# Performance work log

Hardware: AMD Instinct MI355X
Metric: run time of the kernel (lower is better)

Reference implementation:

```python
import jax, jax.numpy as jnp
import numpy as np

N = 262144   # nodes
E = 1048576  # edges (avg degree 4)
DIN = 64     # input node features
H = 128      # hidden channels
DE = 32      # edge feature dim
EPS = 1e-5


def setup_inputs() -> dict:
    key = jax.random.key(0)
    ks = jax.random.split(key, 12)
    s = 0.05
    return {
        "x": jax.random.normal(ks[0], (N, DIN), jnp.float32),
        "edge_attr": jax.random.normal(ks[1], (E, DE), jnp.float32),
        "W_enter": jax.random.normal(ks[2], (H, DIN), jnp.float32) * s,
        "b_enter": jnp.zeros((H,), jnp.float32),
        "W1": jax.random.normal(ks[3], (H, H + DE), jnp.float32) * s,
        "att_l": jax.random.normal(ks[4], (H,), jnp.float32) * s,
        "att_r": jax.random.normal(ks[5], (H,), jnp.float32) * s,
        "W2": jax.random.normal(ks[6], (H, H), jnp.float32) * s,
        "b_conv": jnp.zeros((H,), jnp.float32),
        "W_ih": jax.random.normal(ks[7], (3 * H, H), jnp.float32) * s,
        "W_hh": jax.random.normal(ks[8], (3 * H, H), jnp.float32) * s,
        "b_ih": jnp.zeros((3 * H,), jnp.float32),
        "b_hh": jnp.zeros((3 * H,), jnp.float32),
        "edge_index": jax.random.randint(ks[9], (2, E), 0, N, jnp.int32),
    }


def _segment_softmax(logits, seg, num_segments):
    m = jax.ops.segment_max(logits, seg, num_segments=num_segments)
    e = jnp.exp(logits - m[seg])
    d = jax.ops.segment_sum(e, seg, num_segments=num_segments)
    return e / d[seg]


def reference(x, edge_attr, W_enter, b_enter, W1, att_l, att_r, W2, b_conv,
              W_ih, W_hh, b_ih, b_hh, edge_index):
    n = x.shape[0]
    src, dst = edge_index[0], edge_index[1]  # x_j = x[src], aggregate to dst

    # lin_enter + leaky_relu
    x = jax.nn.leaky_relu(x @ W_enter.T + b_enter)

    # Edge2dConv message: leaky_relu(lin1([x_j, edge_attr]))
    m = jax.nn.leaky_relu(jnp.concatenate([x[src], edge_attr], axis=-1) @ W1.T)  # [E,H]
    alpha = jax.nn.leaky_relu(m @ att_l + x[dst] @ att_r)  # [E]
    alpha = _segment_softmax(alpha, dst, n)
    msg = (m @ W2.T) * alpha[:, None]
    out = jax.ops.segment_sum(msg, dst, num_segments=n) + b_conv

    # elu, then GRUCell(h_in=out_elu, hidden=x)
    h = jax.nn.elu(out)
    gi = h @ W_ih.T + b_ih
    gh = x @ W_hh.T + b_hh
    ir, iz, inn = jnp.split(gi, 3, axis=-1)
    hr, hz, hn = jnp.split(gh, 3, axis=-1)
    r = jax.nn.sigmoid(ir + hr)
    z = jax.nn.sigmoid(iz + hz)
    ncand = jnp.tanh(inn + r * hn)
    x = jax.nn.relu((1.0 - z) * ncand + z * x)

    # layer_norm (no affine)
    mu = jnp.mean(x, axis=-1, keepdims=True)
    var = jnp.mean(jnp.square(x - mu), axis=-1, keepdims=True)
    return (x - mu) / jnp.sqrt(var + EPS)
```

## Files before the change

### kernel.cpp

```cpp
#include <hip/hip_runtime.h>
#include <stdint.h>

#define HD  128
#define DIN 64
#define DE  32

typedef unsigned int u32; typedef unsigned short u16; typedef unsigned char u8;
typedef long i64_;
typedef short s16x8 __attribute__((ext_vector_type(8)));
typedef float f32x4 __attribute__((ext_vector_type(4)));
typedef float f32x2 __attribute__((ext_vector_type(2)));

#define MFMA16(a,b,c)  __builtin_amdgcn_mfma_f32_16x16x32_bf16((a),(b),(c),0,0,0)
#define MFMAF8(a,b,c)  __builtin_amdgcn_mfma_f32_16x16x32_fp8_fp8((a),(b),(c),0,0,0)

__device__ __forceinline__ float lrelu(float x){ return x > 0.f ? x : 0.01f*x; }
__device__ __forceinline__ float sigmoidf_(float x){ return 1.f/(1.f + __expf(-x)); }
__device__ __forceinline__ float tanhf_(float x){
    float t = fminf(fmaxf(x, -15.f), 15.f);
    float e = __expf(2.f*t);
    return (e - 1.f)/(e + 1.f);
}
__device__ __forceinline__ float eluf_(float x){ return x > 0.f ? x : expm1f(x); }

__device__ __forceinline__ u16 f32_to_bf16(float x){
    u32 u = __float_as_uint(x);
    u += 0x7FFFu + ((u >> 16) & 1u);
    return (u16)(u >> 16);
}
__device__ __forceinline__ float bf16lo(u32 u){ return __uint_as_float((u & 0xFFFFu) << 16); }
__device__ __forceinline__ float bf16hi(u32 u){ return __uint_as_float(u & 0xFFFF0000u); }
__device__ __forceinline__ float bf16f(u16 h){ return __uint_as_float(((u32)h) << 16); }
__device__ __forceinline__ u32 pk2(float a, float b){
    return (u32)f32_to_bf16(a) | ((u32)f32_to_bf16(b) << 16);
}
__device__ __forceinline__ u8 hw_f8(float v){
    return (u8)__builtin_amdgcn_cvt_pk_fp8_f32(v, v, 0, false);
}
__device__ __forceinline__ u32 hw_f8x4(float a, float b, float c, float d){
    u32 r = (u32)__builtin_amdgcn_cvt_pk_fp8_f32(a, b, 0, false);
    r = (u32)__builtin_amdgcn_cvt_pk_fp8_f32(c, d, (int)r, true);
    return r;
}
__device__ __forceinline__ f32x2 hw_f8_dec2(u32 u){
    return __builtin_amdgcn_cvt_pk_f32_fp8((int)u, false);
}
__device__ __forceinline__ f32x2 hw_f8_dec2_hi(u32 u){
    return __builtin_amdgcn_cvt_pk_f32_fp8((int)u, true);
}

__device__ __forceinline__ float wave_max(float v){
    #pragma unroll
    for (int o = 32; o > 0; o >>= 1) v = fmaxf(v, __shfl_xor(v, o, 64));
    return v;
}
__device__ __forceinline__ float wave_sum(float v){
    #pragma unroll
    for (int o = 32; o > 0; o >>= 1) v += __shfl_xor(v, o, 64);
    return v;
}

__global__ void k_prep(const float* __restrict__ W1, const float* __restrict__ W2,
                       const float* __restrict__ Went,
                       const float* __restrict__ Wih, const float* __restrict__ Whh,
                       u16* __restrict__ W1b, u16* __restrict__ W2b,
                       u16* __restrict__ Wentb, u8* __restrict__ Bgf8)
{
    int i = blockIdx.x*256 + threadIdx.x;
    if (i < 20480){ W1b[i] = f32_to_bf16(W1[i]); return; }
    i -= 20480;
    if (i < 16384){ W2b[i] = f32_to_bf16(W2[i]); return; }
    i -= 16384;
    if (i < 8192){ Wentb[i] = f32_to_bf16(Went[i]); return; }
    i -= 8192;
    if (i < 131072){
        int col = i >> 8, k = i & 255;
        int g = col >> 7, j = col & 127;
        float v;
        if      (g == 0) v = (k < 128) ? Wih[j*128 + k]        : Whh[j*128 + k - 128];
        else if (g == 1) v = (k < 128) ? Wih[(128+j)*128 + k]  : Whh[(128+j)*128 + k - 128];
        else if (g == 2) v = (k < 128) ? Wih[(256+j)*128 + k]  : 0.f;
        else             v = (k < 128) ? 0.f                   : Whh[(256+j)*128 + k - 128];
        Bgf8[i] = hw_f8(v);
    }
}

__global__ __launch_bounds__(256, 4) void k_enter_mfma(
    const float* __restrict__ x, const u16* __restrict__ Wb, const float* __restrict__ be,
    const float* __restrict__ att_r, u16* __restrict__ xeb, u8* __restrict__ Agru,
    float* __restrict__ r_out, int N)
{
    __shared__ __align__(16) u8 sA[64*144];
    __shared__ __align__(16) u8 sO[64*272];
    int t = threadIdx.x, w = t >> 6, lane = t & 63, l15 = lane & 15, l4 = lane >> 4;
    int tile = blockIdx.x;

    s16x8 bfr[2][2];
    #pragma unroll
    for (int kf = 0; kf < 2; ++kf)
        #pragma unroll
        for (int cf = 0; cf < 2; ++cf)
            bfr[kf][cf] = *(const s16x8*)(Wb + (size_t)(w*32 + cf*16 + l15)*64 + kf*32 + l4*8);

    int el = t >> 2, q = t & 3;
    size_t n = (size_t)tile*64 + el;
    {
        const float4* xs = (const float4*)(x + n*64 + q*16);
        float4 f0 = xs[0], f1 = xs[1], f2 = xs[2], f3 = xs[3];
        uint4 o0, o1;
        o0.x = pk2(f0.x,f0.y); o0.y = pk2(f0.z,f0.w); o0.z = pk2(f1.x,f1.y); o0.w = pk2(f1.z,f1.w);
        o1.x = pk2(f2.x,f2.y); o1.y = pk2(f2.z,f2.w); o1.z = pk2(f3.x,f3.y); o1.w = pk2(f3.z,f3.w);
        *(uint4*)(sA + el*144 + q*32)      = o0;
        *(uint4*)(sA + el*144 + q*32 + 16) = o1;
    }
    __syncthreads();

    f32x4 acc[4][2];
    #pragma unroll
    for (int rf = 0; rf < 4; ++rf){ acc[rf][0] = (f32x4)0.f; acc[rf][1] = (f32x4)0.f; }
    #pragma unroll
    for (int kf = 0; kf < 2; ++kf){
        s16x8 a[4];
        #pragma unroll
        for (int rf = 0; rf < 4; ++rf)
            a[rf] = *(const s16x8*)(sA + (rf*16 + l15)*144 + kf*64 + l4*16);
        #pragma unroll
        for (int rf = 0; rf < 4; ++rf){
            acc[rf][0] = MFMA16(a[rf], bfr[kf][0], acc[rf][0]);
            acc[rf][1] = MFMA16(a[rf], bfr[kf][1], acc[rf][1]);
        }
    }
    float b0 = be[w*32 + l15], b1 = be[w*32 + 16 + l15];
    #pragma unroll
    for (int rf = 0; rf < 4; ++rf)
        #pragma unroll
        for (int r = 0; r < 4; ++r){
            int row = rf*16 + l4*4 + r;
            *(u16*)(sO + row*272 + (w*32 + l15)*2)      = f32_to_bf16(lrelu(acc[rf][0][r] + b0));
            *(u16*)(sO + row*272 + (w*32 + 16 + l15)*2) = f32_to_bf16(lrelu(acc[rf][1][r] + b1));
        }
    __syncthreads();

    float dot = 0.f;
    #pragma unroll
    for (int i = 0; i < 4; ++i){
        uint4 v = *(const uint4*)(sO + el*272 + q*64 + 16*i);
        ((uint4*)xeb)[n*16 + q*4 + i] = v;
        float f0 = bf16lo(v.x), f1 = bf16hi(v.x), f2 = bf16lo(v.y), f3 = bf16hi(v.y);
        float f4 = bf16lo(v.z), f5 = bf16hi(v.z), f6 = bf16lo(v.w), f7 = bf16hi(v.w);
        const float* al = att_r + q*32 + 8*i;
        dot = fmaf(f0, al[0], dot); dot = fmaf(f1, al[1], dot);
        dot = fmaf(f2, al[2], dot); dot = fmaf(f3, al[3], dot);
        dot = fmaf(f4, al[4], dot); dot = fmaf(f5, al[5], dot);
        dot = fmaf(f6, al[6], dot); dot = fmaf(f7, al[7], dot);
        uint2 p; p.x = hw_f8x4(f0, f1, f2, f3); p.y = hw_f8x4(f4, f5, f6, f7);
        *(uint2*)(Agru + n*256 + 128 + q*32 + i*8) = p;
    }
    dot += __shfl_xor(dot, 1); dot += __shfl_xor(dot, 2);
    if (q == 0) r_out[n] = dot;
}

__global__ void k_hist(const int* __restrict__ dst, int* __restrict__ deg, int E){
    int e = blockIdx.x*256 + threadIdx.x;
    if (e < E) atomicAdd(&deg[dst[e]], 1);
}
__global__ __launch_bounds__(256) void k_scan_a(
    const int* __restrict__ deg, int* __restrict__ rs, int* __restrict__ btot, int N)
{
    __shared__ int sd[256];
    int b = blockIdx.x, t = threadIdx.x;
    int base = b*1024 + t*4;
    int d0 = deg[base], d1 = deg[base+1], d2 = deg[base+2], d3 = deg[base+3];
    int s = d0 + d1 + d2 + d3;
    sd[t] = s; __syncthreads();
    for (int o = 1; o < 256; o <<= 1){
        int v = (t >= o) ? sd[t-o] : 0;
        __syncthreads();
        sd[t] += v;
        __syncthreads();
    }
    int ex = sd[t] - s;
    rs[base]   = ex;
    rs[base+1] = ex + d0;
    rs[base+2] = ex + d0 + d1;
    rs[base+3] = ex + d0 + d1 + d2;
    if (t == 0) btot[b] = sd[255];
}
__global__ __launch_bounds__(256) void k_scan_b(const int* __restrict__ btot, int* __restrict__ bbase){
    __shared__ int sd[256];
    int t = threadIdx.x;
    int s = btot[t];
    sd[t] = s; __syncthreads();
    for (int o = 1; o < 256; o <<= 1){
        int v = (t >= o) ? sd[t-o] : 0;
        __syncthreads();
        sd[t] += v;
        __syncthreads();
    }
    bbase[t] = sd[t] - s;
}
__global__ void k_scan_c(int* __restrict__ rs, const int* __restrict__ bbase, int N, int E){
    int i = blockIdx.x*256 + threadIdx.x;
    if (i < N) rs[i] += bbase[i >> 10];
    if (i == 0) rs[N] = E;
}
__global__ void k_scatter(const int* __restrict__ dst, const int* __restrict__ rs,
                          int* __restrict__ cnt, int* __restrict__ epos, int E){
    int e = blockIdx.x*256 + threadIdx.x;
    if (e >= E) return;
    int d = dst[e];
    int pos = rs[d] + atomicAdd(&cnt[d], 1);
    epos[e] = pos;
}

__global__ __launch_bounds__(512, 4) void k_edge_mfma(
    const u16* __restrict__ xeb, const float* __restrict__ ea,
    const u16* __restrict__ W1b, const float* __restrict__ att_l,
    const int* __restrict__ src, const int* __restrict__ epos,
    u8* __restrict__ m, float* __restrict__ alpha, int ntiles, int E)
{
    __shared__ __align__(16) u8 sA[64*336];
    __shared__ __align__(16) u8 sM[64*144];
    int t = threadIdx.x, w = t >> 6, lane = t & 63, l15 = lane & 15, l4 = lane >> 4;

    s16x8 bfr[5];
    #pragma unroll
    for (int kf = 0; kf < 5; ++kf)
        bfr[kf] = *(const s16x8*)(W1b + (size_t)(w*16 + l15)*160 + kf*32 + l4*8);

    int el = t >> 3, q = t & 7;
    int stride = gridDim.x;
    int tile = blockIdx.x;

    uint4 cx0, cx1;
    u32 ce0, ce1;
    int pe = 0;
    {
        int e = tile*64 + el;
        if (tile < ntiles && e < E){
            int sn = src[e];
            const uint4* xs = (const uint4*)xeb + (size_t)sn*16 + q*2;
            cx0 = xs[0]; cx1 = xs[1];
            float4 f = *(const float4*)(ea + (size_t)e*32 + q*4);
            ce0 = pk2(f.x, f.y); ce1 = pk2(f.z, f.w);
            pe  = epos[e];
        }
    }

    int ptile = -1;
    int pe_prev = 0;

    for (; tile < ntiles; tile += stride){
        int e = tile*64 + el;
        if (e < E){
            uint4* d = (uint4*)(sA + el*336 + q*32);
            d[0] = cx0; d[1] = cx1;
            *(u32*)(sA + el*336 + 256 + q*8)     = ce0;
            *(u32*)(sA + el*336 + 256 + q*8 + 4) = ce1;
        }
        int pe_cur = pe;

        int nt = tile + stride;
        if (nt < ntiles){
            int e2 = nt*64 + el;
            if (e2 < E){
                int sn = src[e2];
                const uint4* xs = (const uint4*)xeb + (size_t)sn*16 + q*2;
                cx0 = xs[0]; cx1 = xs[1];
                float4 f = *(const float4*)(ea + (size_t)e2*32 + q*4);
                ce0 = pk2(f.x, f.y); ce1 = pk2(f.z, f.w);
                pe  = epos[e2];
            }
        }

        if (ptile >= 0){
            int ep = ptile*64 + el;
            if (ep < E){
                uint4 v = *(const uint4*)(sM + el*144 + q*16);
                ((uint4*)m)[(size_t)pe_prev*8 + q] = v;
                u32 ws[4] = {v.x, v.y, v.z, v.w};
                float dotv = 0.f;
                #pragma unroll
                for (int i = 0; i < 4; ++i){
                    f32x2 fa = hw_f8_dec2(ws[i]);
                    f32x2 fb = hw_f8_dec2_hi(ws[i]);
                    const float* al = att_l + q*16 + i*4;
                    dotv = fmaf(fa.x, al[0], dotv); dotv = fmaf(fa.y, al[1], dotv);
                    dotv = fmaf(fb.x, al[2], dotv); dotv = fmaf(fb.y, al[3], dotv);
                }
                dotv += __shfl_xor(dotv, 1); dotv += __shfl_xor(dotv, 2); dotv += __shfl_xor(dotv, 4);
                if (q == 0) alpha[pe_prev] = dotv;
            }
        }
        __syncthreads();

        f32x4 acc[4];
        #pragma unroll
        for (int rf = 0; rf < 4; ++rf) acc[rf] = (f32x4)0.f;
        #pragma unroll
        for (int kf = 0; kf < 5; ++kf){
            s16x8 a[4];
            #pragma unroll
            for (int rf = 0; rf < 4; ++rf)
                a[rf] = *(const s16x8*)(sA + (rf*16 + l15)*336 + kf*64 + l4*16);
            #pragma unroll
            for (int rf = 0; rf < 4; ++rf)
                acc[rf] = MFMA16(a[rf], bfr[kf], acc[rf]);
        }

        int col = w*16 + l15;
        #pragma unroll
        for (int rf = 0; rf < 4; ++rf)
            #pragma unroll
            for (int r = 0; r < 4; ++r){
                int row = rf*16 + l4*4 + r;
                sM[row*144 + col] = hw_f8(lrelu(acc[rf][r]));
            }
        __syncthreads();

        ptile = tile; pe_prev = pe_cur;
    }

    if (ptile >= 0){
        int ep = ptile*64 + el;
        if (ep < E){
            uint4 v = *(const uint4*)(sM + el*144 + q*16);
            ((uint4*)m)[(size_t)pe_prev*8 + q] = v;
            u32 ws[4] = {v.x, v.y, v.z, v.w};
            float dotv = 0.f;
            #pragma unroll
            for (int i = 0; i < 4; ++i){
                f32x2 fa = hw_f8_dec2(ws[i]);
                f32x2 fb = hw_f8_dec2_hi(ws[i]);
                const float* al = att_l + q*16 + i*4;
                dotv = fmaf(fa.x, al[0], dotv); dotv = fmaf(fa.y, al[1], dotv);
                dotv = fmaf(fb.x, al[2], dotv); dotv = fmaf(fb.y, al[3], dotv);
            }
            dotv += __shfl_xor(dotv, 1); dotv += __shfl_xor(dotv, 2); dotv += __shfl_xor(dotv, 4);
            if (q == 0) alpha[pe_prev] = dotv;
        }
    }
}

__global__ __launch_bounds__(512, 4) void k_aggconv(
    const int* __restrict__ rs, const float* __restrict__ alpha, const u8* __restrict__ m,
    const float* __restrict__ r_dst,
    const u16* __restrict__ W2b, const float* __restrict__ bc,
    u8* __restrict__ Agru, int N)
{
    __shared__ __align__(16) u8 sA[64*272];
    __shared__ __align__(16) u8 sO[64*272];
    int t = threadIdx.x, w = t >> 6, lane = t & 63, l15 = lane & 15, l4 = lane >> 4;
    int tile = blockIdx.x;

    s16x8 bfr[4];
    #pragma unroll
    for (int kf = 0; kf < 4; ++kf)
        bfr[kf] = *(const s16x8*)(W2b + (size_t)(w*16 + l15)*128 + kf*32 + l4*8);

    #pragma unroll 1
    for (int i = 0; i < 8; ++i){
        int nloc = w*8 + i;
        int n = tile*64 + nloc;
        int s = rs[n], tend = rs[n+1];
        int deg = tend - s;
        float rn = r_dst[n];
        float ax = 0.f, ay = 0.f;
        if (deg > 0 && deg <= 64){
            float av = -1e38f;
            if (lane < deg) av = lrelu(alpha[s + lane] + rn);
            float mx = wave_max(av);
            float ev = (lane < deg) ? __expf(av - mx) : 0.f;
            float ssum = wave_sum(ev);
            float wreg = ev / ssum;
            int k = 0;
            for (; k + 2 <= deg; k += 2){
                float w0 = __shfl(wreg, k);
                float w1 = __shfl(wreg, k + 1);
                u32 u0 = *(const u16*)(m + (size_t)(s + k)*HD + 2*lane);
                u32 u1 = *(const u16*)(m + (size_t)(s + k + 1)*HD + 2*lane);
                f32x2 f0 = hw_f8_dec2(u0);
                f32x2 f1 = hw_f8_dec2(u1);
                ax = fmaf(w0, f0.x, ax); ay = fmaf(w0, f0.y, ay);
                ax = fmaf(w1, f1.x, ax); ay = fmaf(w1, f1.y, ay);
            }
            if (k < deg){
                float w0 = __shfl(wreg, k);
                u32 u0 = *(const u16*)(m + (size_t)(s + k)*HD + 2*lane);
                f32x2 f0 = hw_f8_dec2(u0);
                ax = fmaf(w0, f0.x, ax); ay = fmaf(w0, f0.y, ay);
            }
        } else if (deg > 64){
            float mx = -1e38f;
            for (int k = lane; k < deg; k += 64) mx = fmaxf(mx, lrelu(alpha[s + k] + rn));
            mx = wave_max(mx);
            float ssum = 0.f;
            for (int k = lane; k < deg; k += 64) ssum += __expf(lrelu(alpha[s + k] + rn) - mx);
            ssum = wave_sum(ssum);
            float inv = 1.f / ssum;
            for (int k = 0; k < deg; ++k){
                float wgt = __expf(lrelu(alpha[s + k] + rn) - mx) * inv;
                u32 u0 = *(const u16*)(m + (size_t)(s + k)*HD + 2*lane);
                f32x2 f0 = hw_f8_dec2(u0);
                ax = fmaf(wgt, f0.x, ax);
                ay = fmaf(wgt, f0.y, ay);
            }
        }
        *(u32*)(sA + nloc*272 + lane*4) = pk2(ax, ay);
    }
    __syncthreads();

    f32x4 acc[4];
    #pragma unroll
    for (int rf = 0; rf < 4; ++rf) acc[rf] = (f32x4)0.f;
    #pragma unroll
    for (int kf = 0; kf < 4; ++kf){
        s16x8 av[4];
        #pragma unroll
        for (int rf = 0; rf < 4; ++rf)
            av[rf] = *(const s16x8*)(sA + (rf*16 + l15)*272 + kf*64 + l4*16);
        #pragma unroll
        for (int rf = 0; rf < 4; ++rf)
            acc[rf] = MFMA16(av[rf], bfr[kf], acc[rf]);
    }
    float b0 = bc[w*16 + l15];
    #pragma unroll
    for (int rf = 0; rf < 4; ++rf)
        #pragma unroll
        for (int r = 0; r < 4; ++r){
            int row = rf*16 + l4*4 + r;
            *(u16*)(sO + row*272 + (w*16 + l15)*2) = f32_to_bf16(eluf_(acc[rf][r] + b0));
        }
    __syncthreads();

    {
        int el = t >> 3, q = t & 7;
        size_t n = (size_t)tile*64 + el;
        uint4 v0 = *(const uint4*)(sO + el*272 + q*32);
        uint4 v1 = *(const uint4*)(sO + el*272 + q*32 + 16);
        uint4 p;
        p.x = hw_f8x4(bf16lo(v0.x), bf16hi(v0.x), bf16lo(v0.y), bf16hi(v0.y));
        p.y = hw_f8x4(bf16lo(v0.z), bf16hi(v0.z), bf16lo(v0.w), bf16hi(v0.w));
        p.z = hw_f8x4(bf16lo(v1.x), bf16hi(v1.x), bf16lo(v1.y), bf16hi(v1.y));
        p.w = hw_f8x4(bf16lo(v1.z), bf16hi(v1.z), bf16lo(v1.w), bf16hi(v1.w));
        *(uint4*)(Agru + n*256 + q*16) = p;
    }
}

__global__ __launch_bounds__(512, 4) void k_gru_mfma(
    const u8* __restrict__ Agru, const u16* __restrict__ xeb, const u8* __restrict__ Bgf8,
    const float* __restrict__ bih, const float* __restrict__ bhh,
    float* __restrict__ out, int N, int ntiles)
{
    __shared__ __align__(16) u8 sA[32*272];
    __shared__ __align__(16) u8 sX[32*272];
    __shared__ __align__(16) float sOut[32*132];
    int t = threadIdx.x, w = t >> 6, lane = t & 63, l15 = lane & 15, l4 = lane >> 4;

    i64_ bfr0[8], bfr1[8], bfr2[4], bfr3[4];
    {
        int jc = w*16 + l15;
        #pragma unroll
        for (int kf = 0; kf < 8; ++kf){
            bfr0[kf] = *(const i64_*)(Bgf8 + (size_t)(jc)*256       + kf*32 + l4*8);
            bfr1[kf] = *(const i64_*)(Bgf8 + (size_t)(128 + jc)*256 + kf*32 + l4*8);
        }
        #pragma unroll
        for (int kf = 0; kf < 4; ++kf){
            bfr2[kf] = *(const i64_*)(Bgf8 + (size_t)(256 + jc)*256 + kf*32 + l4*8);
            bfr3[kf] = *(const i64_*)(Bgf8 + (size_t)(384 + jc)*256 + (kf+4)*32 + l4*8);
        }
    }
    int j = w*16 + l15;
    float rb = bih[j] + bhh[j];
    float zb = bih[128 + j] + bhh[128 + j];
    float ib = bih[256 + j];
    float hb = bhh[256 + j];

    int el = t >> 4, part = t & 15;
    int stride = gridDim.x;
    int tile = blockIdx.x;
    uint4 pa, px;
    if (tile < ntiles){
        pa = *((const uint4*)Agru + ((size_t)tile*32 + el)*16 + part);
        px = *((const uint4*)xeb  + ((size_t)tile*32 + el)*16 + part);
    }

    for (; tile < ntiles; tile += stride){
        *(uint4*)(sA + el*272 + part*16) = pa;
        *(uint4*)(sX + el*272 + part*16) = px;
        __syncthreads();

        int nt = tile + stride;
        if (nt < ntiles){
            pa = *((const uint4*)Agru + ((size_t)nt*32 + el)*16 + part);
            px = *((const uint4*)xeb  + ((size_t)nt*32 + el)*16 + part);
        }

        f32x4 acc[2][4];
        #pragma unroll
        for (int rf = 0; rf < 2; ++rf)
            #pragma unroll
            for (int g = 0; g < 4; ++g) acc[rf][g] = (f32x4)0.f;
        #pragma unroll
        for (int kf = 0; kf < 8; ++kf){
            i64_ a0 = *(const i64_*)(sA + l15*272 + kf*32 + l4*8);
            i64_ a1 = *(const i64_*)(sA + (16 + l15)*272 + kf*32 + l4*8);
            acc[0][0] = MFMAF8(a0, bfr0[kf], acc[0][0]);
            acc[1][0] = MFMAF8(a1, bfr0[kf], acc[1][0]);
            acc[0][1] = MFMAF8(a0, bfr1[kf], acc[0][1]);
            acc[1][1] = MFMAF8(a1, bfr1[kf], acc[1][1]);
            if (kf < 4){
                acc[0][2] = MFMAF8(a0, bfr2[kf], acc[0][2]);
                acc[1][2] = MFMAF8(a1, bfr2[kf], acc[1][2]);
            } else {
                acc[0][3] = MFMAF8(a0, bfr3[kf-4], acc[0][3]);
                acc[1][3] = MFMAF8(a1, bfr3[kf-4], acc[1][3]);
            }
        }
        #pragma unroll
        for (int rf = 0; rf < 2; ++rf)
            #pragma unroll
            for (int r = 0; r < 4; ++r){
                int rl = rf*16 + l4*4 + r;
                float rr = sigmoidf_(acc[rf][0][r] + rb);
                float zz = sigmoidf_(acc[rf][1][r] + zb);
                float iv = acc[rf][2][r] + ib;
                float hv = acc[rf][3][r] + hb;
                float nc = tanhf_(iv + rr*hv);
                float xej = bf16f(*(const u16*)(sX + rl*272 + 2*j));
                float v = (1.f - zz)*nc + zz*xej;
                v = fmaxf(v, 0.f);
                sOut[rl*132 + j] = v;
            }
        __syncthreads();
        {
            int row = t >> 4, sub = t & 15;
            const float* rp = sOut + row*132 + sub*8;
            float v0 = rp[0], v1 = rp[1], v2 = rp[2], v3 = rp[3];
            float v4 = rp[4], v5 = rp[5], v6 = rp[6], v7 = rp[7];
            float s1 = v0+v1+v2+v3+v4+v5+v6+v7;
            float s2 = v0*v0+v1*v1+v2*v2+v3*v3+v4*v4+v5*v5+v6*v6+v7*v7;
            #pragma unroll
            for (int o = 1; o < 16; o <<= 1){ s1 += __shfl_xor(s1, o); s2 += __shfl_xor(s2, o); }
            float mu  = s1 * (1.f/128.f);
            float var = s2 * (1.f/128.f) - mu*mu;
            var = fmaxf(var, 0.f);
            float rsd = rsqrtf(var + 1e-5f);
            float* op = out + ((size_t)tile*32 + row)*128 + sub*8;
            float4 o0, o1;
            o0.x = (v0-mu)*rsd; o0.y = (v1-mu)*rsd; o0.z = (v2-mu)*rsd; o0.w = (v3-mu)*rsd;
            o1.x = (v4-mu)*rsd; o1.y = (v5-mu)*rsd; o1.z = (v6-mu)*rsd; o1.w = (v7-mu)*rsd;
            ((float4*)op)[0] = o0; ((float4*)op)[1] = o1;
        }
        __syncthreads();
    }
}

extern "C" void kernel_launch(void* const* d_in, const int* in_sizes, int n_in,
                              void* d_out, int out_size, void* d_ws, size_t ws_size,
                              hipStream_t stream)
{
    const float* x       = (const float*)d_in[0];
    const float* ea      = (const float*)d_in[1];
    const float* W_enter = (const float*)d_in[2];
    const float* b_enter = (const float*)d_in[3];
    const float* W1      = (const float*)d_in[4];
    const float* att_l   = (const float*)d_in[5];
    const float* att_r   = (const float*)d_in[6];
    const float* W2      = (const float*)d_in[7];
    const float* b_conv  = (const float*)d_in[8];
    const float* W_ih    = (const float*)d_in[9];
    const float* W_hh    = (const float*)d_in[10];
    const float* b_ih    = (const float*)d_in[11];
    const float* b_hh    = (const float*)d_in[12];
    const int*   eidx    = (const int*)d_in[13];

    int N = in_sizes[0] / DIN;
    int E = in_sizes[13] / 2;
    const int* src = eidx;
    const int* dst = eidx + E;
    float* out = (float*)d_out;

    size_t off = 0;
    char* base = (char*)d_ws;
    auto alloc = [&](size_t bytes) -> char* {
        char* p = base + off;
        off = (off + bytes + 255) & ~(size_t)255;
        return p;
    };
    u16*   xeb   = (u16*)  alloc((size_t)N*HD*2);
    u8*    Agru  = (u8*)   alloc((size_t)N*256);
    float* r_dst = (float*)alloc((size_t)N*4);
    float* alpha = (float*)alloc((size_t)E*4);
    int*   deg   = (int*)  alloc((size_t)N*4);
    int*   rs    = (int*)  alloc((size_t)(N+1)*4);
    int*   cnt   = (int*)  alloc((size_t)N*4);
    int*   epos  = (int*)  alloc((size_t)E*4);
    int*   btot  = (int*)  alloc(1024);
    int*   bbase = (int*)  alloc(1024);
    u16*   W1b   = (u16*)  alloc(20480*2);
    u16*   W2b   = (u16*)  alloc(16384*2);
    u16*   Wentb = (u16*)  alloc(8192*2);
    u8*    Bgf8  = (u8*)   alloc(131072);
    u8*    mbuf  = (u8*)   alloc((size_t)E*HD);

    int ntiles_n64 = N/64, ntiles_e = (E + 63)/64, ntiles_g = N/32;

    k_prep   <<<(176128+255)/256, 256, 0, stream>>>(W1, W2, W_enter, W_ih, W_hh, W1b, W2b, Wentb, Bgf8);
    hipMemsetAsync(deg, 0, (size_t)N*4, stream);
    hipMemsetAsync(cnt, 0, (size_t)N*4, stream);
    k_enter_mfma<<<ntiles_n64, 256, 0, stream>>>(x, Wentb, b_enter, att_r, xeb, Agru, r_dst, N);
    k_hist   <<<(E+255)/256, 256, 0, stream>>>(dst, deg, E);
    k_scan_a <<<N/1024, 256, 0, stream>>>(deg, rs, btot, N);
    k_scan_b <<<1, 256, 0, stream>>>(btot, bbase);
    k_scan_c <<<(N+255)/256, 256, 0, stream>>>(rs, bbase, N, E);
    k_scatter<<<(E+255)/256, 256, 0, stream>>>(dst, rs, cnt, epos, E);
    k_edge_mfma<<<1024, 512, 0, stream>>>(xeb, ea, W1b, att_l, src, epos,
                                          mbuf, alpha, ntiles_e, E);
    k_aggconv<<<ntiles_n64, 512, 0, stream>>>(rs, alpha, mbuf, r_dst, W2b, b_conv, Agru, N);
    k_gru_mfma  <<<1024, 512, 0, stream>>>(Agru, xeb, Bgf8, b_ih, b_hh, out, N, ntiles_g);
}
```

Before: 510.3 us.

## Fuse aggregation/conv kernel with GRU and layer-norm kernel

Merges the aggregation+W2 kernel with the GRU+layernorm kernel so the ELU output stays in shared memory as fp8 instead of going through a global Agru buffer. The enter kernel now writes a compact fp8 copy of x (Agx) that the fused kernel loads. This removes one kernel launch and a global write/read of the intermediate. In exchange the fused kernel holds more registers and shared memory (launch bounds lowered to 3), loses the persistent-grid prefetch the GRU kernel used, and reloads the GRU weights once per 64-node tile.

```diff
diff --git a/kernel.cpp b/kernel.cpp
--- a/kernel.cpp
+++ b/kernel.cpp
@@ -87,7 +87,7 @@
 
 __global__ __launch_bounds__(256, 4) void k_enter_mfma(
     const float* __restrict__ x, const u16* __restrict__ Wb, const float* __restrict__ be,
-    const float* __restrict__ att_r, u16* __restrict__ xeb, u8* __restrict__ Agru,
+    const float* __restrict__ att_r, u16* __restrict__ xeb, u8* __restrict__ Agx,
     float* __restrict__ r_out, int N)
 {
     __shared__ __align__(16) u8 sA[64*144];
@@ -154,7 +154,7 @@
         dot = fmaf(f4, al[4], dot); dot = fmaf(f5, al[5], dot);
         dot = fmaf(f6, al[6], dot); dot = fmaf(f7, al[7], dot);
         uint2 p; p.x = hw_f8x4(f0, f1, f2, f3); p.y = hw_f8x4(f4, f5, f6, f7);
-        *(uint2*)(Agru + n*256 + 128 + q*32 + i*8) = p;
+        *(uint2*)(Agx + n*128 + q*32 + i*8) = p;
     }
     dot += __shfl_xor(dot, 1); dot += __shfl_xor(dot, 2);
     if (q == 0) r_out[n] = dot;
@@ -342,21 +342,45 @@
     }
 }
 
-__global__ __launch_bounds__(512, 4) void k_aggconv(
+__global__ __launch_bounds__(512, 3) void k_aggconvgru(
     const int* __restrict__ rs, const float* __restrict__ alpha, const u8* __restrict__ m,
     const float* __restrict__ r_dst,
     const u16* __restrict__ W2b, const float* __restrict__ bc,
-    u8* __restrict__ Agru, int N)
+    const u8* __restrict__ Agx, const u16* __restrict__ xeb,
+    const u8* __restrict__ Bgf8,
+    const float* __restrict__ bih, const float* __restrict__ bhh,
+    float* __restrict__ out, int N)
 {
     __shared__ __align__(16) u8 sA[64*272];
     __shared__ __align__(16) u8 sO[64*272];
+    __shared__ __align__(16) float sOut[32*132];
     int t = threadIdx.x, w = t >> 6, lane = t & 63, l15 = lane & 15, l4 = lane >> 4;
     int tile = blockIdx.x;
 
-    s16x8 bfr[4];
+    i64_ bfr0[8], bfr1[8], bfr2[4], bfr3[4];
+    {
+        int jc = w*16 + l15;
+        #pragma unroll
+        for (int kf = 0; kf < 8; ++kf){
+            bfr0[kf] = *(const i64_*)(Bgf8 + (size_t)(jc)*256       + kf*32 + l4*8);
+            bfr1[kf] = *(const i64_*)(Bgf8 + (size_t)(128 + jc)*256 + kf*32 + l4*8);
+        }
+        #pragma unroll
+        for (int kf = 0; kf < 4; ++kf){
+            bfr2[kf] = *(const i64_*)(Bgf8 + (size_t)(256 + jc)*256 + kf*32 + l4*8);
+            bfr3[kf] = *(const i64_*)(Bgf8 + (size_t)(384 + jc)*256 + (kf+4)*32 + l4*8);
+        }
+    }
+    int j = w*16 + l15;
+    float rb = bih[j] + bhh[j];
+    float zb = bih[128 + j] + bhh[128 + j];
+    float ib = bih[256 + j];
+    float hb = bhh[256 + j];
+
+    s16x8 bfrW[4];
     #pragma unroll
     for (int kf = 0; kf < 4; ++kf)
-        bfr[kf] = *(const s16x8*)(W2b + (size_t)(w*16 + l15)*128 + kf*32 + l4*8);
+        bfrW[kf] = *(const s16x8*)(W2b + (size_t)(w*16 + l15)*128 + kf*32 + l4*8);
 
     #pragma unroll 1
     for (int i = 0; i < 8; ++i){
@@ -410,102 +434,54 @@
     }
     __syncthreads();
 
-    f32x4 acc[4];
-    #pragma unroll
-    for (int rf = 0; rf < 4; ++rf) acc[rf] = (f32x4)0.f;
-    #pragma unroll
-    for (int kf = 0; kf < 4; ++kf){
-        s16x8 av[4];
+    int grow = t >> 3, gq = t & 7;
+    size_t gn = (size_t)tile*64 + grow;
+    uint4 gxe  = *((const uint4*)(Agx + gn*128) + gq);
+    uint4 gxb0 = *((const uint4*)(xeb + gn*128) + gq*2);
+    uint4 gxb1 = *((const uint4*)(xeb + gn*128) + gq*2 + 1);
+
+    {
+        f32x4 acc[4];
+        #pragma unroll
+        for (int rf = 0; rf < 4; ++rf) acc[rf] = (f32x4)0.f;
+        #pragma unroll
+        for (int kf = 0; kf < 4; ++kf){
+            s16x8 av[4];
+            #pragma unroll
+            for (int rf = 0; rf < 4; ++rf)
+                av[rf] = *(const s16x8*)(sA + (rf*16 + l15)*272 + kf*64 + l4*16);
+            #pragma unroll
+            for (int rf = 0; rf < 4; ++rf)
+                acc[rf] = MFMA16(av[rf], bfrW[kf], acc[rf]);
+        }
+        float b0 = bc[w*16 + l15];
+        int col = w*16 + l15;
         #pragma unroll
         for (int rf = 0; rf < 4; ++rf)
-            av[rf] = *(const s16x8*)(sA + (rf*16 + l15)*272 + kf*64 + l4*16);
-        #pragma unroll
-        for (int rf = 0; rf < 4; ++rf)
-            acc[rf] = MFMA16(av[rf], bfr[kf], acc[rf]);
-    }
-    float b0 = bc[w*16 + l15];
-    #pragma unroll
-    for (int rf = 0; rf < 4; ++rf)
-        #pragma unroll
-        for (int r = 0; r < 4; ++r){
-            int row = rf*16 + l4*4 + r;
-            *(u16*)(sO + row*272 + (w*16 + l15)*2) = f32_to_bf16(eluf_(acc[rf][r] + b0));
-        }
+            #pragma unroll
+            for (int r = 0; r < 4; ++r){
+                int row = rf*16 + l4*4 + r;
+                sO[row*272 + col] = hw_f8(bf16f(f32_to_bf16(eluf_(acc[rf][r] + b0))));
+            }
+    }
+    *(uint4*)(sO + grow*272 + 128 + gq*16) = gxe;
     __syncthreads();
 
-    {
-        int el = t >> 3, q = t & 7;
-        size_t n = (size_t)tile*64 + el;
-        uint4 v0 = *(const uint4*)(sO + el*272 + q*32);
-        uint4 v1 = *(const uint4*)(sO + el*272 + q*32 + 16);
-        uint4 p;
-        p.x = hw_f8x4(bf16lo(v0.x), bf16hi(v0.x), bf16lo(v0.y), bf16hi(v0.y));
-        p.y = hw_f8x4(bf16lo(v0.z), bf16hi(v0.z), bf16lo(v0.w), bf16hi(v0.w));
-        p.z = hw_f8x4(bf16lo(v1.x), bf16hi(v1.x), bf16lo(v1.y), bf16hi(v1.y));
-        p.w = hw_f8x4(bf16lo(v1.z), bf16hi(v1.z), bf16lo(v1.w), bf16hi(v1.w));
-        *(uint4*)(Agru + n*256 + q*16) = p;
-    }
-}
-
-__global__ __launch_bounds__(512, 4) void k_gru_mfma(
-    const u8* __restrict__ Agru, const u16* __restrict__ xeb, const u8* __restrict__ Bgf8,
-    const float* __restrict__ bih, const float* __restrict__ bhh,
-    float* __restrict__ out, int N, int ntiles)
-{
-    __shared__ __align__(16) u8 sA[32*272];
-    __shared__ __align__(16) u8 sX[32*272];
-    __shared__ __align__(16) float sOut[32*132];
-    int t = threadIdx.x, w = t >> 6, lane = t & 63, l15 = lane & 15, l4 = lane >> 4;
-
-    i64_ bfr0[8], bfr1[8], bfr2[4], bfr3[4];
-    {
-        int jc = w*16 + l15;
+    *(uint4*)(sA + grow*272 + gq*32)      = gxb0;
+    *(uint4*)(sA + grow*272 + gq*32 + 16) = gxb1;
+    __syncthreads();
+
+    #pragma unroll 1
+    for (int hh = 0; hh < 2; ++hh){
+        f32x4 acc[2][4];
+        #pragma unroll
+        for (int rf = 0; rf < 2; ++rf)
+            #pragma unroll
+            for (int g = 0; g < 4; ++g) acc[rf][g] = (f32x4)0.f;
         #pragma unroll
         for (int kf = 0; kf < 8; ++kf){
-            bfr0[kf] = *(const i64_*)(Bgf8 + (size_t)(jc)*256       + kf*32 + l4*8);
-            bfr1[kf] = *(const i64_*)(Bgf8 + (size_t)(128 + jc)*256 + kf*32 + l4*8);
-        }
-        #pragma unroll
-        for (int kf = 0; kf < 4; ++kf){
-            bfr2[kf] = *(const i64_*)(Bgf8 + (size_t)(256 + jc)*256 + kf*32 + l4*8);
-            bfr3[kf] = *(const i64_*)(Bgf8 + (size_t)(384 + jc)*256 + (kf+4)*32 + l4*8);
-        }
-    }
-    int j = w*16 + l15;
-    float rb = bih[j] + bhh[j];
-    float zb = bih[128 + j] + bhh[128 + j];
-    float ib = bih[256 + j];
-    float hb = bhh[256 + j];
-
-    int el = t >> 4, part = t & 15;
-    int stride = gridDim.x;
-    int tile = blockIdx.x;
-    uint4 pa, px;
-    if (tile < ntiles){
-        pa = *((const uint4*)Agru + ((size_t)tile*32 + el)*16 + part);
-        px = *((const uint4*)xeb  + ((size_t)tile*32 + el)*16 + part);
-    }
-
-    for (; tile < ntiles; tile += stride){
-        *(uint4*)(sA + el*272 + part*16) = pa;
-        *(uint4*)(sX + el*272 + part*16) = px;
-        __syncthreads();
-
-        int nt = tile + stride;
-        if (nt < ntiles){
-            pa = *((const uint4*)Agru + ((size_t)nt*32 + el)*16 + part);
-            px = *((const uint4*)xeb  + ((size_t)nt*32 + el)*16 + part);
-        }
-
-        f32x4 acc[2][4];
-        #pragma unroll
-        for (int rf = 0; rf < 2; ++rf)
-            #pragma unroll
-            for (int g = 0; g < 4; ++g) acc[rf][g] = (f32x4)0.f;
-        #pragma unroll
-        for (int kf = 0; kf < 8; ++kf){
-            i64_ a0 = *(const i64_*)(sA + l15*272 + kf*32 + l4*8);
-            i64_ a1 = *(const i64_*)(sA + (16 + l15)*272 + kf*32 + l4*8);
+            i64_ a0 = *(const i64_*)(sO + (hh*32 + l15)*272 + kf*32 + l4*8);
+            i64_ a1 = *(const i64_*)(sO + (hh*32 + 16 + l15)*272 + kf*32 + l4*8);
             acc[0][0] = MFMAF8(a0, bfr0[kf], acc[0][0]);
             acc[1][0] = MFMAF8(a1, bfr0[kf], acc[1][0]);
             acc[0][1] = MFMAF8(a0, bfr1[kf], acc[0][1]);
@@ -528,7 +504,7 @@
                 float iv = acc[rf][2][r] + ib;
                 float hv = acc[rf][3][r] + hb;
                 float nc = tanhf_(iv + rr*hv);
-                float xej = bf16f(*(const u16*)(sX + rl*272 + 2*j));
+                float xej = bf16f(*(const u16*)(sA + (hh*32 + rl)*272 + 2*j));
                 float v = (1.f - zz)*nc + zz*xej;
                 v = fmaxf(v, 0.f);
                 sOut[rl*132 + j] = v;
@@ -547,7 +523,7 @@
             float var = s2 * (1.f/128.f) - mu*mu;
             var = fmaxf(var, 0.f);
             float rsd = rsqrtf(var + 1e-5f);
-            float* op = out + ((size_t)tile*32 + row)*128 + sub*8;
+            float* op = out + ((size_t)tile*64 + hh*32 + row)*128 + sub*8;
             float4 o0, o1;
             o0.x = (v0-mu)*rsd; o0.y = (v1-mu)*rsd; o0.z = (v2-mu)*rsd; o0.w = (v3-mu)*rsd;
             o1.x = (v4-mu)*rsd; o1.y = (v5-mu)*rsd; o1.z = (v6-mu)*rsd; o1.w = (v7-mu)*rsd;
@@ -590,7 +566,7 @@
         return p;
     };
     u16*   xeb   = (u16*)  alloc((size_t)N*HD*2);
-    u8*    Agru  = (u8*)   alloc((size_t)N*256);
+    u8*    Agx   = (u8*)   alloc((size_t)N*HD);
     float* r_dst = (float*)alloc((size_t)N*4);
     float* alpha = (float*)alloc((size_t)E*4);
     int*   deg   = (int*)  alloc((size_t)N*4);
@@ -605,12 +581,12 @@
     u8*    Bgf8  = (u8*)   alloc(131072);
     u8*    mbuf  = (u8*)   alloc((size_t)E*HD);
 
-    int ntiles_n64 = N/64, ntiles_e = (E + 63)/64, ntiles_g = N/32;
+    int ntiles_n64 = N/64, ntiles_e = (E + 63)/64;
 
     k_prep   <<<(176128+255)/256, 256, 0, stream>>>(W1, W2, W_enter, W_ih, W_hh, W1b, W2b, Wentb, Bgf8);
     hipMemsetAsync(deg, 0, (size_t)N*4, stream);
     hipMemsetAsync(cnt, 0, (size_t)N*4, stream);
-    k_enter_mfma<<<ntiles_n64, 256, 0, stream>>>(x, Wentb, b_enter, att_r, xeb, Agru, r_dst, N);
+    k_enter_mfma<<<ntiles_n64, 256, 0, stream>>>(x, Wentb, b_enter, att_r, xeb, Agx, r_dst, N);
     k_hist   <<<(E+255)/256, 256, 0, stream>>>(dst, deg, E);
     k_scan_a <<<N/1024, 256, 0, stream>>>(deg, rs, btot, N);
     k_scan_b <<<1, 256, 0, stream>>>(btot, bbase);
@@ -618,6 +594,6 @@
     k_scatter<<<(E+255)/256, 256, 0, stream>>>(dst, rs, cnt, epos, E);
     k_edge_mfma<<<1024, 512, 0, stream>>>(xeb, ea, W1b, att_l, src, epos,
                                           mbuf, alpha, ntiles_e, E);
-    k_aggconv<<<ntiles_n64, 512, 0, stream>>>(rs, alpha, mbuf, r_dst, W2b, b_conv, Agru, N);
-    k_gru_mfma  <<<1024, 512, 0, stream>>>(Agru, xeb, Bgf8, b_ih, b_hh, out, N, ntiles_g);
-}
+    k_aggconvgru<<<ntiles_n64, 512, 0, stream>>>(rs, alpha, mbuf, r_dst, W2b, b_conv,
+                                                 Agx, xeb, Bgf8, b_ih, b_hh, out, N);
+}
```

Measured after the change: 621.8 us. 1.22x slower.
